# Kernel tuning notes

Measured on AMD Instinct MI355X. Metric: run time of the kernel, lower is better.

## Reference

```python
import jax, jax.numpy as jnp
import numpy as np

H_SIZE = 4096
N_HEADS = 32
N_KV = 8
HEAD_DIM = H_SIZE // N_HEADS  # 128
GROUP = N_HEADS // N_KV       # 4 (GQA)
Q_SIZE = N_HEADS * HEAD_DIM
KV_SIZE = N_KV * HEAD_DIM
SCALE = HEAD_DIM ** -0.5
NUM_SEQS = 64
MAX_CTX = 2048
BLOCK_SIZE = 16
BLOCKS_PER_SEQ = MAX_CTX // BLOCK_SIZE  # 128
NUM_BLOCKS = NUM_SEQS * BLOCKS_PER_SEQ  # 8192
ROPE_THETA = 10000.0


def apply_rope(x, positions):
    # x: [S, H, D], positions: [S] int. GPT-NeoX style rotate-half RoPE.
    half = HEAD_DIM // 2
    inv_freq = 1.0 / (ROPE_THETA ** (jnp.arange(0, half, dtype=jnp.float32) / half))
    angles = positions.astype(jnp.float32)[:, None] * inv_freq[None, :]  # [S, half]
    cos = jnp.cos(angles)[:, None, :]  # [S, 1, half]
    sin = jnp.sin(angles)[:, None, :]
    x1, x2 = x[..., :half], x[..., half:]
    return jnp.concatenate([x1 * cos - x2 * sin, x2 * cos + x1 * sin], axis=-1)


def setup_inputs() -> dict:
    key = jax.random.key(0)
    ks = jax.random.split(key, 8)
    context_lens = jax.random.randint(ks[0], (NUM_SEQS,), 1, MAX_CTX + 1)
    positions = context_lens - 1  # decode: current token at position ctx-1
    hidden_states = jax.random.normal(ks[1], (NUM_SEQS, H_SIZE), jnp.float32)
    k_cache = jax.random.normal(ks[2], (NUM_BLOCKS, BLOCK_SIZE, N_KV, HEAD_DIM), jnp.float32)
    v_cache = jax.random.normal(ks[3], (NUM_BLOCKS, BLOCK_SIZE, N_KV, HEAD_DIM), jnp.float32)
    # non-contiguous block assignment, each block used once
    block_tables = jax.random.permutation(ks[4], NUM_BLOCKS).reshape(NUM_SEQS, BLOCKS_PER_SEQ)
    W_qkv = jax.random.normal(ks[5], (Q_SIZE + 2 * KV_SIZE, H_SIZE), jnp.float32) * 0.02
    W_o = jax.random.normal(ks[6], (H_SIZE, Q_SIZE), jnp.float32) * 0.02
    return {"positions": positions, "hidden_states": hidden_states,
            "k_cache": k_cache, "v_cache": v_cache,
            "block_tables": block_tables, "context_lens": context_lens,
            "W_qkv": W_qkv, "W_o": W_o}


def reference(positions, hidden_states, k_cache, v_cache, block_tables, context_lens, W_qkv, W_o):
    S = hidden_states.shape[0]
    # fused QKV projection (bias-free, torch Linear convention: x @ W.T)
    qkv = hidden_states @ W_qkv.T  # [S, (H+2K)*D]
    q = qkv[:, :Q_SIZE].reshape(S, N_HEADS, HEAD_DIM)
    k = qkv[:, Q_SIZE:Q_SIZE + KV_SIZE].reshape(S, N_KV, HEAD_DIM)
    v = qkv[:, Q_SIZE + KV_SIZE:].reshape(S, N_KV, HEAD_DIM)
    # RoPE on q and the new k (cached keys are stored post-rotation)
    q = apply_rope(q, positions)
    k = apply_rope(k, positions)
    # gather paged KV via block tables -> [S, MAX_CTX, KV, D]
    keys = k_cache[block_tables].reshape(S, MAX_CTX, N_KV, HEAD_DIM)
    vals = v_cache[block_tables].reshape(S, MAX_CTX, N_KV, HEAD_DIM)
    pos_idx = jnp.arange(MAX_CTX)
    is_cur = pos_idx[None, :] == positions[:, None]  # [S, L] slot of current token
    keys = jnp.where(is_cur[:, :, None, None], k[:, None], keys)
    vals = jnp.where(is_cur[:, :, None, None], v[:, None], vals)
    # GQA attention: q grouped as [S, KV, GROUP, D]
    qg = q.reshape(S, N_KV, GROUP, HEAD_DIM)
    scores = jnp.einsum('skgd,slkd->skgl', qg, keys) * SCALE  # [S, KV, G, L]
    valid = pos_idx[None, :] < context_lens[:, None]          # [S, L]
    scores = jnp.where(valid[:, None, None, :], scores, jnp.finfo(scores.dtype).min)
    probs = jax.nn.softmax(scores, axis=-1)
    attn = jnp.einsum('skgl,slkd->skgd', probs, vals).reshape(S, Q_SIZE)
    return attn @ W_o.T  # [S, H_SIZE]
```

## Files before the change

kernel.cpp:

```cpp
#include <hip/hip_runtime.h>
#include <math.h>

#define H_SIZE   4096
#define N_HEADS  32
#define N_KV     8
#define HEAD_DIM 128
#define GROUP    4
#define Q_SIZE   4096
#define KV_SIZE  1024
#define QKV_OUT  6144
#define NUM_SEQS 64
#define MAX_CTX  2048
#define BLK_SZ   16
#define BLOCKS_PER_SEQ 128
#define ATT_SCALE 0.08838834764831845f

#define CHUNK    128
#define NCHUNK   16
#define KSPLIT   8
#define KCHUNK   512

typedef __attribute__((ext_vector_type(8))) short bf16x8;
typedef __attribute__((ext_vector_type(4))) float f32x4;

__device__ __forceinline__ short f2bf(float f) {
    return __builtin_bit_cast(short, (__bf16)f);
}

__device__ __forceinline__ bf16x8 cvt8(float4 a, float4 b) {
    bf16x8 r;
    r[0]=f2bf(a.x); r[1]=f2bf(a.y); r[2]=f2bf(a.z); r[3]=f2bf(a.w);
    r[4]=f2bf(b.x); r[5]=f2bf(b.y); r[6]=f2bf(b.z); r[7]=f2bf(b.w);
    return r;
}

__global__ __launch_bounds__(256)
void cvt_bf16(const float* __restrict__ in, unsigned short* __restrict__ out, int n4) {
    int i = blockIdx.x * 256 + threadIdx.x;
    if (i >= n4) return;
    float4 v = *(const float4*)(in + (size_t)i * 4);
    ushort2 lo = { (unsigned short)f2bf(v.x), (unsigned short)f2bf(v.y) };
    ushort2 hi = { (unsigned short)f2bf(v.z), (unsigned short)f2bf(v.w) };
    *(ushort2*)(out + (size_t)i * 4)     = lo;
    *(ushort2*)(out + (size_t)i * 4 + 2) = hi;
}

__global__ __launch_bounds__(256)
void gemm_mfma(const unsigned short* __restrict__ A, const float* __restrict__ W,
               float* __restrict__ Yp, int N) {
    const int n0   = blockIdx.x * 64;
    const int k0   = blockIdx.y * KCHUNK;
    const int wave = threadIdx.x >> 6;
    const int lane = threadIdx.x & 63;
    const int ncol = n0 + wave * 16 + (lane & 15);
    const int klane = (lane >> 4) * 8;

    const float*          wrow = W + (size_t)ncol * H_SIZE + k0 + klane;
    const unsigned short* arow = A + (size_t)(lane & 15) * H_SIZE + k0 + klane;

    f32x4 acc[4] = {};
    for (int k = 0; k < KCHUNK; k += 32) {
        float4 wa = *(const float4*)(wrow + k);
        float4 wb = *(const float4*)(wrow + k + 4);
        bf16x8 bf = cvt8(wa, wb);
        #pragma unroll
        for (int m = 0; m < 4; ++m) {
            bf16x8 af = *(const bf16x8*)(const void*)(arow + (size_t)m * 16 * H_SIZE + k);
            acc[m] = __builtin_amdgcn_mfma_f32_16x16x32_bf16(af, bf, acc[m], 0, 0, 0);
        }
    }
    float* yp = Yp + (size_t)blockIdx.y * 64 * N;
    #pragma unroll
    for (int m = 0; m < 4; ++m)
        #pragma unroll
        for (int j = 0; j < 4; ++j)
            yp[(size_t)(m * 16 + (lane >> 4) * 4 + j) * N + ncol] = acc[m][j];
}

__global__ __launch_bounds__(256)
void qkv_reduce_rope(const float* __restrict__ Yp, float* __restrict__ qkv,
                     const int* __restrict__ positions) {
    const int s   = blockIdx.x;
    const int idx = blockIdx.y * 256 + threadIdx.x;
    const float pos = (float)positions[s];
    if (idx < 2560) {
        const int head = idx >> 6, d = idx & 63;
        const int j1 = (head < N_HEADS ? head * HEAD_DIM
                                       : Q_SIZE + (head - N_HEADS) * HEAD_DIM) + d;
        const int j2 = j1 + 64;
        float x1 = 0.f, x2 = 0.f;
        #pragma unroll
        for (int c = 0; c < KSPLIT; ++c) {
            x1 += Yp[((size_t)c * 64 + s) * QKV_OUT + j1];
            x2 += Yp[((size_t)c * 64 + s) * QKV_OUT + j2];
        }
        const float inv_freq = powf(10000.0f, -(float)d / 64.0f);
        const float ang = pos * inv_freq;
        const float cs = cosf(ang), sn = sinf(ang);
        qkv[(size_t)s * QKV_OUT + j1] = x1 * cs - x2 * sn;
        qkv[(size_t)s * QKV_OUT + j2] = x2 * cs + x1 * sn;
    } else if (idx < 3584) {
        const int j = Q_SIZE + KV_SIZE + (idx - 2560);
        float v = 0.f;
        #pragma unroll
        for (int c = 0; c < KSPLIT; ++c)
            v += Yp[((size_t)c * 64 + s) * QKV_OUT + j];
        qkv[(size_t)s * QKV_OUT + j] = v;
    }
}

__global__ __launch_bounds__(256)
void reduce_ksplit(const float* __restrict__ Yp, float* __restrict__ Y, int total) {
    int i = blockIdx.x * 256 + threadIdx.x;
    if (i >= total) return;
    float s = 0.f;
    #pragma unroll
    for (int c = 0; c < KSPLIT; ++c) s += Yp[(size_t)c * total + i];
    Y[i] = s;
}

__global__ __launch_bounds__(256)
void attn_chunk(const float* __restrict__ qkv,
                const float* __restrict__ k_cache,
                const float* __restrict__ v_cache,
                const int*   __restrict__ block_tables,
                const int*   __restrict__ context_lens,
                float* __restrict__ pacc,
                float* __restrict__ pml) {
    const int sh = blockIdx.x;
    const int s  = sh >> 3;
    const int h  = sh & 7;
    const int c  = blockIdx.y;
    const int ctx = context_lens[s];
    if (c * CHUNK >= ctx) return;
    const int pos = ctx - 1;
    const int nv = min(CHUNK, ctx - c * CHUNK);

    __shared__ float qs[GROUP][HEAD_DIM];
    __shared__ float sc[GROUP][CHUNK];
    __shared__ float red[4][GROUP][HEAD_DIM];

    const int tid  = threadIdx.x;
    const int w    = tid >> 6;
    const int lane = tid & 63;

    {
        int i = tid * 2;
        const float* qsrc = qkv + (size_t)s * QKV_OUT + h * (GROUP * HEAD_DIM);
        *(float2*)(&qs[i >> 7][i & 127]) = *(const float2*)(qsrc + i);
    }
    __syncthreads();

    const int*   bt   = block_tables + s * BLOCKS_PER_SEQ;
    const float* ksec = qkv + (size_t)s * QKV_OUT + Q_SIZE + h * HEAD_DIM;
    const float* vsec = qkv + (size_t)s * QKV_OUT + Q_SIZE + KV_SIZE + h * HEAD_DIM;

    const int blk0 = bt[c * (CHUNK / BLK_SZ) + w * 2];
    const int blk1 = bt[c * (CHUNK / BLK_SZ) + w * 2 + 1];

    {
        const int tk   = w * 32 + (lane >> 1);
        const int half = lane & 1;
        const int T    = c * CHUNK + tk;
        const int blk  = (lane < 32) ? blk0 : blk1;
        const float* kp = (T == pos) ? ksec
            : k_cache + ((size_t)(blk * BLK_SZ + (tk & 15)) * N_KV + h) * HEAD_DIM;
        kp += half * 64;
        const float* q0 = &qs[0][half * 64];
        const float* q1 = &qs[1][half * 64];
        const float* q2 = &qs[2][half * 64];
        const float* q3 = &qs[3][half * 64];
        float d0 = 0.f, d1 = 0.f, d2 = 0.f, d3 = 0.f;
        #pragma unroll
        for (int b = 0; b < 2; ++b) {
            float4 kv[8];
            #pragma unroll
            for (int j = 0; j < 8; ++j) kv[j] = *(const float4*)(kp + b * 32 + j * 4);
            #pragma unroll
            for (int j = 0; j < 8; ++j) {
                const float4 A = kv[j];
                const float4 x0 = *(const float4*)(q0 + b * 32 + j * 4);
                const float4 x1 = *(const float4*)(q1 + b * 32 + j * 4);
                const float4 x2 = *(const float4*)(q2 + b * 32 + j * 4);
                const float4 x3 = *(const float4*)(q3 + b * 32 + j * 4);
                d0 = fmaf(A.x,x0.x, fmaf(A.y,x0.y, fmaf(A.z,x0.z, fmaf(A.w,x0.w, d0))));
                d1 = fmaf(A.x,x1.x, fmaf(A.y,x1.y, fmaf(A.z,x1.z, fmaf(A.w,x1.w, d1))));
                d2 = fmaf(A.x,x2.x, fmaf(A.y,x2.y, fmaf(A.z,x2.z, fmaf(A.w,x2.w, d2))));
                d3 = fmaf(A.x,x3.x, fmaf(A.y,x3.y, fmaf(A.z,x3.z, fmaf(A.w,x3.w, d3))));
            }
        }
        d0 += __shfl_xor(d0, 1);
        d1 += __shfl_xor(d1, 1);
        d2 += __shfl_xor(d2, 1);
        d3 += __shfl_xor(d3, 1);
        if (half == 0) {
            const bool v = (tk < nv);
            sc[0][tk] = v ? d0 * ATT_SCALE : -1e30f;
            sc[1][tk] = v ? d1 * ATT_SCALE : -1e30f;
            sc[2][tk] = v ? d2 * ATT_SCALE : -1e30f;
            sc[3][tk] = v ? d3 * ATT_SCALE : -1e30f;
        }
    }
    __syncthreads();

    {
        const int g = w;
        const float v0 = sc[g][lane];
        const float v1 = sc[g][lane + 64];
        float m = fmaxf(v0, v1);
        #pragma unroll
        for (int off = 32; off; off >>= 1) m = fmaxf(m, __shfl_xor(m, off));
        const float e0 = __expf(v0 - m);
        const float e1 = __expf(v1 - m);
        float l = e0 + e1;
        #pragma unroll
        for (int off = 32; off; off >>= 1) l += __shfl_xor(l, off);
        sc[g][lane]      = e0;
        sc[g][lane + 64] = e1;
        if (lane == 0) {
            size_t ib = (((size_t)sh * NCHUNK + c) * GROUP + g) * 2;
            pml[ib] = m; pml[ib + 1] = l;
        }
    }
    __syncthreads();

    {
        const int t0 = w * 32;
        const float* vb0 = v_cache + (size_t)blk0 * (BLK_SZ * N_KV * HEAD_DIM)
                         + (size_t)h * HEAD_DIM + lane * 2;
        const float* vb1 = v_cache + (size_t)blk1 * (BLK_SZ * N_KV * HEAD_DIM)
                         + (size_t)h * HEAD_DIM + lane * 2;
        const float* vnewp = vsec + lane * 2;
        float2 a0 = {0,0}, a1 = {0,0}, a2 = {0,0}, a3 = {0,0};
        #pragma unroll
        for (int tb = 0; tb < 32; tb += 8) {
            float2 vv[8];
            #pragma unroll
            for (int u = 0; u < 8; ++u) {
                const int tt = tb + u;
                const float* vp = (c * CHUNK + t0 + tt == pos) ? vnewp
                    : ((tt < 16 ? vb0 : vb1) + (size_t)(tt & 15) * (N_KV * HEAD_DIM));
                vv[u] = *(const float2*)vp;
            }
            #pragma unroll
            for (int u = 0; u < 8; ++u) {
                const int tk = t0 + tb + u;
                const float p0 = sc[0][tk], p1 = sc[1][tk], p2 = sc[2][tk], p3 = sc[3][tk];
                a0.x = fmaf(p0, vv[u].x, a0.x); a0.y = fmaf(p0, vv[u].y, a0.y);
                a1.x = fmaf(p1, vv[u].x, a1.x); a1.y = fmaf(p1, vv[u].y, a1.y);
                a2.x = fmaf(p2, vv[u].x, a2.x); a2.y = fmaf(p2, vv[u].y, a2.y);
                a3.x = fmaf(p3, vv[u].x, a3.x); a3.y = fmaf(p3, vv[u].y, a3.y);
            }
        }
        *(float2*)(&red[w][0][lane * 2]) = a0;
        *(float2*)(&red[w][1][lane * 2]) = a1;
        *(float2*)(&red[w][2][lane * 2]) = a2;
        *(float2*)(&red[w][3][lane * 2]) = a3;
    }
    __syncthreads();

    {
        const int g = tid >> 6, d = (tid & 63) * 2;
        float2 o = {0.f, 0.f};
        #pragma unroll
        for (int ww = 0; ww < 4; ++ww) {
            o.x += red[ww][g][d];
            o.y += red[ww][g][d + 1];
        }
        size_t ob = (((size_t)sh * NCHUNK + c) * GROUP + g) * HEAD_DIM + d;
        *(float2*)(pacc + ob) = o;
    }
}

__global__ __launch_bounds__(256)
void attn_reduce(const float* __restrict__ pacc, const float* __restrict__ pml,
                 const int* __restrict__ context_lens, unsigned short* __restrict__ outbf) {
    const int sh = blockIdx.x;
    const int s  = sh >> 3;
    const int h  = sh & 7;
    const int g    = threadIdx.x >> 6;
    const int lane = threadIdx.x & 63;
    const int ctx = context_lens[s];
    const int nc  = (ctx + CHUNK - 1) / CHUNK;

    float M = -1e30f;
    for (int cc = 0; cc < nc; ++cc)
        M = fmaxf(M, pml[(((size_t)sh * NCHUNK + cc) * GROUP + g) * 2]);
    float ox = 0.f, oy = 0.f, L = 0.f;
    for (int cc = 0; cc < nc; ++cc) {
        size_t idx = ((size_t)sh * NCHUNK + cc) * GROUP + g;
        float w = __expf(pml[idx*2] - M);
        L = fmaf(w, pml[idx*2+1], L);
        float2 pa = *(const float2*)(pacc + idx * HEAD_DIM + lane*2);
        ox = fmaf(w, pa.x, ox);
        oy = fmaf(w, pa.y, oy);
    }
    float inv = 1.0f / L;
    unsigned short* op = outbf + (size_t)s * Q_SIZE + (h * GROUP + g) * HEAD_DIM;
    ushort2 o2 = { (unsigned short)f2bf(ox * inv), (unsigned short)f2bf(oy * inv) };
    *(ushort2*)(op + lane * 2) = o2;
}

extern "C" void kernel_launch(void* const* d_in, const int* in_sizes, int n_in,
                              void* d_out, int out_size, void* d_ws, size_t ws_size,
                              hipStream_t stream) {
    const int*   positions    = (const int*)  d_in[0];
    const float* hidden       = (const float*)d_in[1];
    const float* k_cache      = (const float*)d_in[2];
    const float* v_cache      = (const float*)d_in[3];
    const int*   block_tables = (const int*)  d_in[4];
    const int*   context_lens = (const int*)  d_in[5];
    const float* W_qkv        = (const float*)d_in[6];
    const float* W_o          = (const float*)d_in[7];
    float* out = (float*)d_out;

    float* qkv_ws = (float*)d_ws;
    unsigned short* hidden_bf = (unsigned short*)(qkv_ws + (size_t)NUM_SEQS * QKV_OUT);
    unsigned short* attn_bf   = hidden_bf + (size_t)NUM_SEQS * H_SIZE;
    float* scratch = (float*)(attn_bf + (size_t)NUM_SEQS * H_SIZE);
    float* pacc = scratch;
    float* pml  = scratch + (size_t)NUM_SEQS * N_KV * NCHUNK * GROUP * HEAD_DIM;

    cvt_bf16<<<(NUM_SEQS * H_SIZE / 4 + 255) / 256, 256, 0, stream>>>(
        hidden, hidden_bf, NUM_SEQS * H_SIZE / 4);
    gemm_mfma<<<dim3(QKV_OUT / 64, KSPLIT), 256, 0, stream>>>(hidden_bf, W_qkv, scratch, QKV_OUT);
    qkv_reduce_rope<<<dim3(NUM_SEQS, 14), 256, 0, stream>>>(scratch, qkv_ws, positions);
    attn_chunk<<<dim3(NUM_SEQS * N_KV, NCHUNK), 256, 0, stream>>>(
        qkv_ws, k_cache, v_cache, block_tables, context_lens, pacc, pml);
    attn_reduce<<<NUM_SEQS * N_KV, 256, 0, stream>>>(pacc, pml, context_lens, attn_bf);
    gemm_mfma<<<dim3(Q_SIZE / 64, KSPLIT), 256, 0, stream>>>(attn_bf, W_o, scratch, Q_SIZE);
    reduce_ksplit<<<(NUM_SEQS * Q_SIZE + 255) / 256, 256, 0, stream>>>(scratch, out, NUM_SEQS * Q_SIZE);
}
```

Measured before the change: 226.8 us.

## Keep softmax scores in registers with per-wave online softmax, dropping two barriers

Each wave now computes max and sum over its own 32 tokens with cross-lane shuffles and keeps the probabilities in registers. The PV loop broadcasts them with __shfl instead of reading a shared score array. The four per-wave partials are rescaled and merged in the final reduction using per-wave max and sum kept in shared memory. This removes the score buffer and two __syncthreads. In exchange it adds many shuffles inside the PV inner loop and extra exp calls in the merge.

```diff
diff --git a/kernel.cpp b/kernel.cpp
--- a/kernel.cpp
+++ b/kernel.cpp
@@ -137,8 +137,9 @@
     const int nv = min(CHUNK, ctx - c * CHUNK);
 
     __shared__ float qs[GROUP][HEAD_DIM];
-    __shared__ float sc[GROUP][CHUNK];
     __shared__ float red[4][GROUP][HEAD_DIM];
+    __shared__ float mw[4][GROUP];
+    __shared__ float lw[4][GROUP];
 
     const int tid  = threadIdx.x;
     const int w    = tid >> 6;
@@ -158,6 +159,7 @@
     const int blk0 = bt[c * (CHUNK / BLK_SZ) + w * 2];
     const int blk1 = bt[c * (CHUNK / BLK_SZ) + w * 2 + 1];
 
+    float p0, p1, p2, p3;
     {
         const int tk   = w * 32 + (lane >> 1);
         const int half = lane & 1;
@@ -193,36 +195,37 @@
         d1 += __shfl_xor(d1, 1);
         d2 += __shfl_xor(d2, 1);
         d3 += __shfl_xor(d3, 1);
-        if (half == 0) {
-            const bool v = (tk < nv);
-            sc[0][tk] = v ? d0 * ATT_SCALE : -1e30f;
-            sc[1][tk] = v ? d1 * ATT_SCALE : -1e30f;
-            sc[2][tk] = v ? d2 * ATT_SCALE : -1e30f;
-            sc[3][tk] = v ? d3 * ATT_SCALE : -1e30f;
-        }
-    }
-    __syncthreads();
-
-    {
-        const int g = w;
-        const float v0 = sc[g][lane];
-        const float v1 = sc[g][lane + 64];
-        float m = fmaxf(v0, v1);
-        #pragma unroll
-        for (int off = 32; off; off >>= 1) m = fmaxf(m, __shfl_xor(m, off));
-        const float e0 = __expf(v0 - m);
-        const float e1 = __expf(v1 - m);
-        float l = e0 + e1;
-        #pragma unroll
-        for (int off = 32; off; off >>= 1) l += __shfl_xor(l, off);
-        sc[g][lane]      = e0;
-        sc[g][lane + 64] = e1;
+        const bool vmask = (tk < nv);
+        float s0 = vmask ? d0 * ATT_SCALE : -1e30f;
+        float s1 = vmask ? d1 * ATT_SCALE : -1e30f;
+        float s2 = vmask ? d2 * ATT_SCALE : -1e30f;
+        float s3 = vmask ? d3 * ATT_SCALE : -1e30f;
+        float m0 = s0, m1 = s1, m2 = s2, m3 = s3;
+        #pragma unroll
+        for (int off = 2; off <= 32; off <<= 1) {
+            m0 = fmaxf(m0, __shfl_xor(m0, off));
+            m1 = fmaxf(m1, __shfl_xor(m1, off));
+            m2 = fmaxf(m2, __shfl_xor(m2, off));
+            m3 = fmaxf(m3, __shfl_xor(m3, off));
+        }
+        p0 = __expf(s0 - m0);
+        p1 = __expf(s1 - m1);
+        p2 = __expf(s2 - m2);
+        p3 = __expf(s3 - m3);
+        float l0 = p0, l1 = p1, l2 = p2, l3 = p3;
+        #pragma unroll
+        for (int off = 2; off <= 32; off <<= 1) {
+            l0 += __shfl_xor(l0, off);
+            l1 += __shfl_xor(l1, off);
+            l2 += __shfl_xor(l2, off);
+            l3 += __shfl_xor(l3, off);
+        }
         if (lane == 0) {
-            size_t ib = (((size_t)sh * NCHUNK + c) * GROUP + g) * 2;
-            pml[ib] = m; pml[ib + 1] = l;
-        }
-    }
-    __syncthreads();
+            mw[w][0] = m0; mw[w][1] = m1; mw[w][2] = m2; mw[w][3] = m3;
+            lw[w][0] = l0; lw[w][1] = l1;
+            lw[w][2] = l2; lw[w][3] = l3;
+        }
+    }
 
     {
         const int t0 = w * 32;
@@ -244,12 +247,15 @@
             }
             #pragma unroll
             for (int u = 0; u < 8; ++u) {
-                const int tk = t0 + tb + u;
-                const float p0 = sc[0][tk], p1 = sc[1][tk], p2 = sc[2][tk], p3 = sc[3][tk];
-                a0.x = fmaf(p0, vv[u].x, a0.x); a0.y = fmaf(p0, vv[u].y, a0.y);
-                a1.x = fmaf(p1, vv[u].x, a1.x); a1.y = fmaf(p1, vv[u].y, a1.y);
-                a2.x = fmaf(p2, vv[u].x, a2.x); a2.y = fmaf(p2, vv[u].y, a2.y);
-                a3.x = fmaf(p3, vv[u].x, a3.x); a3.y = fmaf(p3, vv[u].y, a3.y);
+                const int tt = tb + u;
+                const float q0 = __shfl(p0, 2 * tt);
+                const float q1 = __shfl(p1, 2 * tt);
+                const float q2 = __shfl(p2, 2 * tt);
+                const float q3 = __shfl(p3, 2 * tt);
+                a0.x = fmaf(q0, vv[u].x, a0.x); a0.y = fmaf(q0, vv[u].y, a0.y);
+                a1.x = fmaf(q1, vv[u].x, a1.x); a1.y = fmaf(q1, vv[u].y, a1.y);
+                a2.x = fmaf(q2, vv[u].x, a2.x); a2.y = fmaf(q2, vv[u].y, a2.y);
+                a3.x = fmaf(q3, vv[u].x, a3.x); a3.y = fmaf(q3, vv[u].y, a3.y);
             }
         }
         *(float2*)(&red[w][0][lane * 2]) = a0;
@@ -261,14 +267,21 @@
 
     {
         const int g = tid >> 6, d = (tid & 63) * 2;
-        float2 o = {0.f, 0.f};
-        #pragma unroll
-        for (int ww = 0; ww < 4; ++ww) {
-            o.x += red[ww][g][d];
-            o.y += red[ww][g][d + 1];
-        }
+        const float m0 = mw[0][g], m1 = mw[1][g], m2 = mw[2][g], m3 = mw[3][g];
+        float M = fmaxf(fmaxf(m0, m1), fmaxf(m2, m3));
+        const float e0 = __expf(m0 - M), e1 = __expf(m1 - M);
+        const float e2 = __expf(m2 - M), e3 = __expf(m3 - M);
+        float ox = red[0][g][d]   * e0 + red[1][g][d]   * e1
+                 + red[2][g][d]   * e2 + red[3][g][d]   * e3;
+        float oy = red[0][g][d+1] * e0 + red[1][g][d+1] * e1
+                 + red[2][g][d+1] * e2 + red[3][g][d+1] * e3;
         size_t ob = (((size_t)sh * NCHUNK + c) * GROUP + g) * HEAD_DIM + d;
-        *(float2*)(pacc + ob) = o;
+        *(float2*)(pacc + ob) = make_float2(ox, oy);
+        if ((tid & 63) == 0) {
+            const float L = lw[0][g] * e0 + lw[1][g] * e1 + lw[2][g] * e2 + lw[3][g] * e3;
+            size_t ib = (((size_t)sh * NCHUNK + c) * GROUP + g) * 2;
+            pml[ib] = M; pml[ib + 1] = L;
+        }
     }
 }
 
```

New measurement: 233.3 us. +2.9%, slower.
